# Kernel optimization log

Measured on AMD Instinct MI355X. Metric: run time of the kernel, lower is better.

The kernel has to match this reference:

```python
import jax, jax.numpy as jnp
import numpy as np

N_NODES = 100000
N_EDGES = 3200000
N_GRAPHS = 256
IN_DIM = 128
HID = 64
K = 3


def setup_inputs() -> dict:
    key = jax.random.key(0)
    ks = jax.random.split(key, 10)
    x = jax.random.normal(ks[0], (N_NODES, IN_DIM), dtype=jnp.float32)
    edge_index = jax.random.randint(ks[1], (2, N_EDGES), 0, N_NODES, dtype=jnp.int64)
    batch = jnp.sort(jax.random.randint(ks[2], (N_NODES,), 0, N_GRAPHS, dtype=jnp.int64))
    # ChebConv k-order weights: list of Linear(in, out) -> stacked [K, in, out]
    s1 = 1.0 / np.sqrt(IN_DIM)
    s2 = 1.0 / np.sqrt(HID)
    W1 = jax.random.uniform(ks[3], (K, IN_DIM, HID), jnp.float32, -s1, s1)
    b1 = jax.random.uniform(ks[4], (HID,), jnp.float32, -s1, s1)
    W2 = jax.random.uniform(ks[5], (K, HID, HID), jnp.float32, -s2, s2)
    b2 = jax.random.uniform(ks[6], (HID,), jnp.float32, -s2, s2)
    Wfc = jax.random.uniform(ks[7], (HID, 1), jnp.float32, -s2, s2)
    bfc = jax.random.uniform(ks[8], (1,), jnp.float32, -s2, s2)
    return {"x": x, "edge_index": edge_index, "batch": batch,
            "W1": W1, "b1": b1, "W2": W2, "b2": b2, "Wfc": Wfc, "bfc": bfc}


def _cheb_conv(x, src, dst, edge_w, W, b):
    # PyG ChebConv, sym normalization, lambda_max=2 => L_hat has zero diagonal
    # and off-diagonal -D^{-1/2} A D^{-1/2} (edge_w precomputed, negative).
    n = x.shape[0]
    def lhat(v):  # (L_hat v)_i = sum_{edges j->i} edge_w * v_j
        return jax.ops.segment_sum(edge_w[:, None] * v[src], dst, num_segments=n)
    Tx0 = x
    Tx1 = lhat(Tx0)
    Tx2 = 2.0 * lhat(Tx1) - Tx0
    return Tx0 @ W[0] + Tx1 @ W[1] + Tx2 @ W[2] + b


def reference(x, edge_index, batch, W1, b1, W2, b2, Wfc, bfc):
    src, dst = edge_index[0], edge_index[1]
    n = x.shape[0]
    # degree on row (source), sym normalization
    deg = jax.ops.segment_sum(jnp.ones_like(src, dtype=x.dtype), src, num_segments=n)
    dinv = jnp.where(deg > 0, jax.lax.rsqrt(jnp.maximum(deg, 1.0)), 0.0)
    edge_w = -dinv[src] * dinv[dst]  # scaled Laplacian off-diagonal weights

    h = jax.nn.relu(_cheb_conv(x, src, dst, edge_w, W1, b1))
    h = jax.nn.relu(_cheb_conv(h, src, dst, edge_w, W2, b2))

    # global mean pool over graphs
    sums = jax.ops.segment_sum(h, batch, num_segments=N_GRAPHS)
    counts = jax.ops.segment_sum(jnp.ones((n,), dtype=h.dtype), batch, num_segments=N_GRAPHS)
    pooled = sums / jnp.maximum(counts, 1.0)[:, None]

    return (pooled @ Wfc + bfc).squeeze(-1)  # [N_GRAPHS]
```

## Files before the change

### kernel.cpp

```cpp
#include <hip/hip_runtime.h>
#include <hip/hip_fp16.h>
#include <cstdint>
#include <cstddef>

static constexpr int NN = 100000;
static constexpr int NE = 3200000;
static constexpr int NG = 256;
static constexpr int NBK = (NN + 127) / 128;
static constexpr int EPB = NE / 256;

typedef _Float16 h8 __attribute__((ext_vector_type(8)));
typedef float f4v __attribute__((ext_vector_type(4)));

__device__ __forceinline__ void atomAddF(float* p, float v) {
  unsafeAtomicAdd(p, v);
}

__device__ __forceinline__ float h2f(__half h) { return __half2float(h); }

__device__ __forceinline__ unsigned pk2(float a, float b) {
  unsigned lo = __half_as_ushort(__float2half_rn(a));
  unsigned hi = __half_as_ushort(__float2half_rn(b));
  return lo | (hi << 16);
}

__global__ void k_detect(const int* __restrict__ ei, int* __restrict__ flag) {
  if (threadIdx.x == 0 && blockIdx.x == 0) {
    int nz = 0;
    for (int i = 0; i < 64; ++i) nz += (ei[2 * i + 1] != 0) ? 1 : 0;
    *flag = (nz == 0) ? 1 : 0;
  }
}

__device__ __forceinline__ int ld_idx(const void* raw, int f, int i) {
  return f ? (int)((const long long*)raw)[i] : ((const int*)raw)[i];
}

__global__ __launch_bounds__(256) void k_repack_batch(const void* __restrict__ raw,
                                                      const int* __restrict__ flag,
                                                      int* __restrict__ b32,
                                                      int* __restrict__ gcnt) {
  __shared__ int cnt[256];
  int t = threadIdx.x;
  cnt[t] = 0;
  int blk0 = blockIdx.x * 256;
  int f = *flag;
  int g0 = ld_idx(raw, f, blk0);
  __syncthreads();
  int i = blk0 + t;
  if (i < NN) {
    int g = ld_idx(raw, f, i);
    b32[i] = g;
    atomicAdd(&cnt[g - g0], 1);
  }
  __syncthreads();
  if (cnt[t] > 0) atomicAdd(&gcnt[g0 + t], cnt[t]);
}

__global__ __launch_bounds__(256) void k_hist(const void* __restrict__ raw,
                                              const int* __restrict__ flag,
                                              int* __restrict__ sCnt,
                                              int* __restrict__ dCnt,
                                              int* __restrict__ hsBlk,
                                              int* __restrict__ hdBlk) {
  __shared__ int hs[NBK], hd[NBK];
  int t = threadIdx.x;
  for (int i = t; i < NBK; i += 256) { hs[i] = 0; hd[i] = 0; }
  __syncthreads();
  int f = *flag;
  int e0 = blockIdx.x * EPB;
  for (int e = e0 + t; e < e0 + EPB; e += 256) {
    int s = ld_idx(raw, f, e);
    int d = ld_idx(raw, f, NE + e);
    atomicAdd(&hs[s >> 7], 1);
    atomicAdd(&hd[d >> 7], 1);
  }
  __syncthreads();
  size_t hb = (size_t)blockIdx.x * NBK;
  for (int i = t; i < NBK; i += 256) {
    int a = hs[i], b = hd[i];
    hsBlk[hb + i] = a;
    hdBlk[hb + i] = b;
    if (a) atomicAdd(&sCnt[i], a);
    if (b) atomicAdd(&dCnt[i], b);
  }
}

__global__ __launch_bounds__(1024) void k_scan(const int* __restrict__ sCnt,
                                               const int* __restrict__ dCnt,
                                               int* __restrict__ sBase,
                                               int* __restrict__ dBase,
                                               int* __restrict__ sCur,
                                               int* __restrict__ dCur) {
  __shared__ int sh1[1024], sh2[1024];
  int t = threadIdx.x;
  int v1 = (t < NBK) ? sCnt[t] : 0;
  int v2 = (t < NBK) ? dCnt[t] : 0;
  sh1[t] = v1; sh2[t] = v2;
  __syncthreads();
  for (int off = 1; off < 1024; off <<= 1) {
    int a1 = (t >= off) ? sh1[t - off] : 0;
    int a2 = (t >= off) ? sh2[t - off] : 0;
    __syncthreads();
    sh1[t] += a1; sh2[t] += a2;
    __syncthreads();
  }
  if (t <= NBK) {
    int b1 = sh1[t] - v1, b2 = sh2[t] - v2;
    sBase[t] = b1; dBase[t] = b2;
    if (t < NBK) { sCur[t] = b1; dCur[t] = b2; }
  }
}

__global__ __launch_bounds__(256) void k_scatter(const void* __restrict__ raw,
                                                 const int* __restrict__ flag,
                                                 const int* __restrict__ hsBlk,
                                                 const int* __restrict__ hdBlk,
                                                 int* __restrict__ sCur,
                                                 int* __restrict__ dCur,
                                                 int* __restrict__ srclist,
                                                 unsigned* __restrict__ elist) {
  __shared__ int hs[NBK], hd[NBK], cbS[NBK], cbD[NBK];
  int t = threadIdx.x;
  size_t hb = (size_t)blockIdx.x * NBK;
  for (int i = t; i < NBK; i += 256) {
    int c1 = hsBlk[hb + i];
    cbS[i] = c1 ? atomicAdd(&sCur[i], c1) : 0;
    int c2 = hdBlk[hb + i];
    cbD[i] = c2 ? atomicAdd(&dCur[i], c2) : 0;
    hs[i] = 0; hd[i] = 0;
  }
  __syncthreads();
  int f = *flag;
  int e0 = blockIdx.x * EPB;
  for (int e = e0 + t; e < e0 + EPB; e += 256) {
    int s = ld_idx(raw, f, e);
    int d = ld_idx(raw, f, NE + e);
    int bs = s >> 7, bd = d >> 7;
    int ls = atomicAdd(&hs[bs], 1);
    int ld2 = atomicAdd(&hd[bd], 1);
    srclist[cbS[bs] + ls] = s;
    elist[cbD[bd] + ld2] = (unsigned)s | ((unsigned)(d & 127) << 17);
  }
}

__global__ __launch_bounds__(256) void k_deg(const int* __restrict__ sBase,
                                             const int* __restrict__ srclist,
                                             float* __restrict__ dinv) {
  __shared__ int cnt[128];
  int t = threadIdx.x;
  if (t < 128) cnt[t] = 0;
  __syncthreads();
  int b = blockIdx.x;
  int e0 = sBase[b], e1 = sBase[b + 1];
  for (int i = e0 + t; i < e1; i += 256) atomicAdd(&cnt[srclist[i] & 127], 1);
  __syncthreads();
  if (t < 128) {
    int node = b * 128 + t;
    if (node < NN) {
      int c = cnt[t];
      dinv[node] = (c > 0) ? rsqrtf((float)c) : 0.f;
    }
  }
}

__global__ __launch_bounds__(256) void k_csr(const int* __restrict__ dBase,
                                             const unsigned* __restrict__ elist,
                                             int* __restrict__ rowptr,
                                             int* __restrict__ adj) {
  __shared__ int cnt[128], sc[128], off[128], fill[128];
  int t = threadIdx.x;
  if (t < 128) { cnt[t] = 0; fill[t] = 0; }
  __syncthreads();
  int b = blockIdx.x;
  int e0 = dBase[b], e1 = dBase[b + 1];
  for (int i = e0 + t; i < e1; i += 256) atomicAdd(&cnt[elist[i] >> 17], 1);
  __syncthreads();
  if (t < 128) sc[t] = cnt[t];
  __syncthreads();
  for (int o = 1; o < 128; o <<= 1) {
    int a = (t < 128 && t >= o) ? sc[t - o] : 0;
    __syncthreads();
    if (t < 128) sc[t] += a;
    __syncthreads();
  }
  if (t < 128) {
    off[t] = sc[t] - cnt[t];
    int node = b * 128 + t;
    if (node < NN) rowptr[node] = e0 + off[t];
  }
  if (b == NBK - 1 && t == 0) rowptr[NN] = e1;
  __syncthreads();
  for (int i = e0 + t; i < e1; i += 256) {
    unsigned w2 = elist[i];
    int l = (int)(w2 >> 17);
    int pos = atomicAdd(&fill[l], 1);
    adj[e0 + off[l] + pos] = (int)(w2 & 0x1FFFFu);
  }
}

__global__ __launch_bounds__(256) void k_prepW(const float* __restrict__ W1,
                                               const float* __restrict__ W2,
                                               __half* __restrict__ BtX,
                                               __half* __restrict__ BtH) {
  int t = blockIdx.x * 256 + threadIdx.x;
  if (t < 192 * 128) {
    int n = t >> 7, k = t & 127;
    float v;
    if (n < 64)       v = W1[k * 64 + n] - W1[16384 + k * 64 + n];
    else if (n < 128) v = W1[8192 + k * 64 + (n - 64)];
    else              v = W1[16384 + k * 64 + (n - 128)];
    BtX[n * 128 + k] = __float2half_rn(v);
  } else if (t < 192 * 128 + 64 * 192) {
    int u = t - 192 * 128;
    int n = u / 192, k = u % 192;
    int s = k >> 6, kk = k & 63;
    float v = (s == 0) ? (W2[kk * 64 + n] - W2[8192 + kk * 64 + n])
            : (s == 1) ? W2[4096 + kk * 64 + n]
                       : 2.f * W2[8192 + kk * 64 + n];
    BtH[n * 192 + k] = __float2half_rn(v);
  }
}

static constexpr int AW = 136;
__global__ __launch_bounds__(256) void k_gemm_x(const float* __restrict__ x,
                                                const __half* __restrict__ BtX,
                                                const float* __restrict__ dinv,
                                                __half* __restrict__ gV0,
                                                unsigned* __restrict__ p01) {
  __shared__ __align__(16) _Float16 As[128 * AW];
  const int t = threadIdx.x;
  const int n0 = blockIdx.x * 128;
  {
    int i = t >> 1, q = t & 1;
    int row = n0 + i;
    _Float16* dst = As + i * AW + q * 64;
    if (row < NN) {
      const float* src = x + (size_t)row * 128 + q * 64;
#pragma unroll
      for (int c = 0; c < 64; c += 4) {
        float4 v = *reinterpret_cast<const float4*>(src + c);
        ushort4 u;
        u.x = __half_as_ushort(__float2half_rn(v.x));
        u.y = __half_as_ushort(__float2half_rn(v.y));
        u.z = __half_as_ushort(__float2half_rn(v.z));
        u.w = __half_as_ushort(__float2half_rn(v.w));
        *reinterpret_cast<ushort4*>(dst + c) = u;
      }
    } else {
#pragma unroll
      for (int c = 0; c < 64; c += 4)
        *reinterpret_cast<ushort4*>(dst + c) = make_ushort4(0, 0, 0, 0);
    }
  }
  __syncthreads();
  const int w = t >> 6, lane = t & 63;
  const int quad = lane >> 4, l = lane & 15;
  f4v acc[2][12];
#pragma unroll
  for (int mt = 0; mt < 2; ++mt)
#pragma unroll
    for (int nt = 0; nt < 12; ++nt) acc[mt][nt] = (f4v){0.f, 0.f, 0.f, 0.f};

#pragma unroll
  for (int ks = 0; ks < 4; ++ks) {
    int k0 = ks * 32 + quad * 8;
    h8 a0 = *reinterpret_cast<const h8*>(As + (w * 32 + l) * AW + k0);
    h8 a1 = *reinterpret_cast<const h8*>(As + (w * 32 + 16 + l) * AW + k0);
#pragma unroll
    for (int nt = 0; nt < 12; ++nt) {
      h8 b = *reinterpret_cast<const h8*>(BtX + (size_t)(nt * 16 + l) * 128 + k0);
      acc[0][nt] = __builtin_amdgcn_mfma_f32_16x16x32_f16(a0, b, acc[0][nt], 0, 0, 0);
      acc[1][nt] = __builtin_amdgcn_mfma_f32_16x16x32_f16(a1, b, acc[1][nt], 0, 0, 0);
    }
  }
#pragma unroll
  for (int mt = 0; mt < 2; ++mt) {
#pragma unroll
    for (int r = 0; r < 4; ++r) {
      int row = n0 + w * 32 + mt * 16 + quad * 4 + r;
      if (row < NN) {
        float dv = dinv[row];
#pragma unroll
        for (int nt2 = 0; nt2 < 4; ++nt2) {
          gV0[(size_t)row * 64 + nt2 * 16 + l] = __float2half_rn(acc[mt][nt2][r]);
          p01[(size_t)row * 64 + nt2 * 16 + l] =
              pk2(dv * acc[mt][4 + nt2][r], dv * acc[mt][8 + nt2][r]);
        }
      }
    }
  }
}

__global__ __launch_bounds__(256) void k_prop2p(const int* __restrict__ rp,
                                                const int* __restrict__ adj,
                                                const unsigned* __restrict__ vp,
                                                const float* __restrict__ dinv,
                                                __half* __restrict__ oA,
                                                __half* __restrict__ oB) {
  int node = blockIdx.x * 4 + (threadIdx.x >> 6);
  int d = threadIdx.x & 63;
  if (node >= NN) return;
  int p0 = rp[node], p1 = rp[node + 1];
  float a0 = 0.f, a1 = 0.f, a2 = 0.f, a3 = 0.f;
  float b0 = 0.f, b1 = 0.f, b2 = 0.f, b3 = 0.f;
  union { unsigned u; __half2 h; } cv;
  int p = p0;
  int pA = (p0 + 3) & ~3;
  if (pA > p1) pA = p1;
  for (; p < pA; ++p) {
    cv.u = vp[(size_t)adj[p] * 64 + d];
    float2 f = __half22float2(cv.h);
    a0 += f.x; b0 += f.y;
  }
  for (; p + 8 <= p1; p += 8) {
    int4 e0 = *reinterpret_cast<const int4*>(adj + p);
    int4 e1 = *reinterpret_cast<const int4*>(adj + p + 4);
    unsigned u0 = vp[(size_t)e0.x * 64 + d], u1 = vp[(size_t)e0.y * 64 + d];
    unsigned u2 = vp[(size_t)e0.z * 64 + d], u3 = vp[(size_t)e0.w * 64 + d];
    unsigned u4 = vp[(size_t)e1.x * 64 + d], u5 = vp[(size_t)e1.y * 64 + d];
    unsigned u6 = vp[(size_t)e1.z * 64 + d], u7 = vp[(size_t)e1.w * 64 + d];
    cv.u = u0; { float2 f = __half22float2(cv.h); a0 += f.x; b0 += f.y; }
    cv.u = u1; { float2 f = __half22float2(cv.h); a1 += f.x; b1 += f.y; }
    cv.u = u2; { float2 f = __half22float2(cv.h); a2 += f.x; b2 += f.y; }
    cv.u = u3; { float2 f = __half22float2(cv.h); a3 += f.x; b3 += f.y; }
    cv.u = u4; { float2 f = __half22float2(cv.h); a0 += f.x; b0 += f.y; }
    cv.u = u5; { float2 f = __half22float2(cv.h); a1 += f.x; b1 += f.y; }
    cv.u = u6; { float2 f = __half22float2(cv.h); a2 += f.x; b2 += f.y; }
    cv.u = u7; { float2 f = __half22float2(cv.h); a3 += f.x; b3 += f.y; }
  }
  if (p + 4 <= p1) {
    int4 e = *reinterpret_cast<const int4*>(adj + p);
    unsigned u0 = vp[(size_t)e.x * 64 + d], u1 = vp[(size_t)e.y * 64 + d];
    unsigned u2 = vp[(size_t)e.z * 64 + d], u3 = vp[(size_t)e.w * 64 + d];
    cv.u = u0; { float2 f = __half22float2(cv.h); a0 += f.x; b0 += f.y; }
    cv.u = u1; { float2 f = __half22float2(cv.h); a1 += f.x; b1 += f.y; }
    cv.u = u2; { float2 f = __half22float2(cv.h); a2 += f.x; b2 += f.y; }
    cv.u = u3; { float2 f = __half22float2(cv.h); a3 += f.x; b3 += f.y; }
    p += 4;
  }
  for (; p < p1; ++p) {
    cv.u = vp[(size_t)adj[p] * 64 + d];
    float2 f = __half22float2(cv.h);
    a1 += f.x; b1 += f.y;
  }
  float sa = (a0 + a1) + (a2 + a3);
  float sb = (b0 + b1) + (b2 + b3);
  float dv = dinv[node];
  oA[(size_t)node * 64 + d] = __float2half_rn(-dv * sa);
  oB[(size_t)node * 64 + d] = __float2half_rn(-dv * dv * sb);
}

__global__ __launch_bounds__(256) void k_prop1(const int* __restrict__ rp,
                                               const int* __restrict__ adj,
                                               const __half* __restrict__ vin,
                                               const float* __restrict__ dinv,
                                               __half* __restrict__ o_p,
                                               __half* __restrict__ o_s) {
  int node = blockIdx.x * 4 + (threadIdx.x >> 6);
  int d = threadIdx.x & 63;
  if (node >= NN) return;
  int p0 = rp[node], p1 = rp[node + 1];
  float a0 = 0.f, a1 = 0.f, a2 = 0.f, a3 = 0.f;
  int p = p0;
  int pA = (p0 + 3) & ~3;
  if (pA > p1) pA = p1;
  for (; p < pA; ++p) a0 += h2f(vin[(size_t)adj[p] * 64 + d]);
  for (; p + 8 <= p1; p += 8) {
    int4 e0 = *reinterpret_cast<const int4*>(adj + p);
    int4 e1 = *reinterpret_cast<const int4*>(adj + p + 4);
    a0 += h2f(vin[(size_t)e0.x * 64 + d]);
    a1 += h2f(vin[(size_t)e0.y * 64 + d]);
    a2 += h2f(vin[(size_t)e0.z * 64 + d]);
    a3 += h2f(vin[(size_t)e0.w * 64 + d]);
    a0 += h2f(vin[(size_t)e1.x * 64 + d]);
    a1 += h2f(vin[(size_t)e1.y * 64 + d]);
    a2 += h2f(vin[(size_t)e1.z * 64 + d]);
    a3 += h2f(vin[(size_t)e1.w * 64 + d]);
  }
  if (p + 4 <= p1) {
    int4 e = *reinterpret_cast<const int4*>(adj + p);
    a0 += h2f(vin[(size_t)e.x * 64 + d]);
    a1 += h2f(vin[(size_t)e.y * 64 + d]);
    a2 += h2f(vin[(size_t)e.z * 64 + d]);
    a3 += h2f(vin[(size_t)e.w * 64 + d]);
    p += 4;
  }
  for (; p < p1; ++p) a1 += h2f(vin[(size_t)adj[p] * 64 + d]);
  float s = (a0 + a1) + (a2 + a3);
  float dv = dinv[node];
  float pl = -dv * s;
  o_p[(size_t)node * 64 + d] = __float2half_rn(pl);
  if (o_s) o_s[(size_t)node * 64 + d] = __float2half_rn(dv * pl);
}

__global__ __launch_bounds__(256) void k_prop_h1(const int* __restrict__ rp,
                                                 const int* __restrict__ adj,
                                                 const __half* __restrict__ vin,
                                                 const float* __restrict__ dinv,
                                                 const __half* __restrict__ gV0,
                                                 const __half* __restrict__ gP,
                                                 const float* __restrict__ b1v,
                                                 __half* __restrict__ gH1,
                                                 __half* __restrict__ gH1s) {
  int node = blockIdx.x * 4 + (threadIdx.x >> 6);
  int d = threadIdx.x & 63;
  if (node >= NN) return;
  int p0 = rp[node], p1 = rp[node + 1];
  float a0 = 0.f, a1 = 0.f, a2 = 0.f, a3 = 0.f;
  int p = p0;
  int pA = (p0 + 3) & ~3;
  if (pA > p1) pA = p1;
  for (; p < pA; ++p) a0 += h2f(vin[(size_t)adj[p] * 64 + d]);
  for (; p + 8 <= p1; p += 8) {
    int4 e0 = *reinterpret_cast<const int4*>(adj + p);
    int4 e1 = *reinterpret_cast<const int4*>(adj + p + 4);
    a0 += h2f(vin[(size_t)e0.x * 64 + d]);
    a1 += h2f(vin[(size_t)e0.y * 64 + d]);
    a2 += h2f(vin[(size_t)e0.z * 64 + d]);
    a3 += h2f(vin[(size_t)e0.w * 64 + d]);
    a0 += h2f(vin[(size_t)e1.x * 64 + d]);
    a1 += h2f(vin[(size_t)e1.y * 64 + d]);
    a2 += h2f(vin[(size_t)e1.z * 64 + d]);
    a3 += h2f(vin[(size_t)e1.w * 64 + d]);
  }
  if (p + 4 <= p1) {
    int4 e = *reinterpret_cast<const int4*>(adj + p);
    a0 += h2f(vin[(size_t)e.x * 64 + d]);
    a1 += h2f(vin[(size_t)e.y * 64 + d]);
    a2 += h2f(vin[(size_t)e.z * 64 + d]);
    a3 += h2f(vin[(size_t)e.w * 64 + d]);
    p += 4;
  }
  for (; p < p1; ++p) a1 += h2f(vin[(size_t)adj[p] * 64 + d]);
  float s = (a0 + a1) + (a2 + a3);
  float dv = dinv[node];
  float R = -dv * s;
  size_t idx = (size_t)node * 64 + d;
  float h = h2f(gV0[idx]) + h2f(gP[idx]) + 2.f * R + b1v[d];
  h = fmaxf(h, 0.f);
  gH1[idx] = __float2half_rn(h);
  gH1s[idx] = __float2half_rn(dv * h);
}

static constexpr int HW = 200;
__global__ __launch_bounds__(256) void k_gemm_h2_pool(const __half* __restrict__ gH1,
                                                      const __half* __restrict__ gT1,
                                                      const __half* __restrict__ gT2,
                                                      const __half* __restrict__ BtH,
                                                      const float* __restrict__ b2v,
                                                      const int* __restrict__ b32,
                                                      float* __restrict__ pooled) {
  __shared__ __align__(16) char smem[128 * HW * 2];
  __shared__ int gb[128];
  _Float16* As = reinterpret_cast<_Float16*>(smem);
  const int t = threadIdx.x;
  const int n0 = blockIdx.x * 128;
  if (t < 128) gb[t] = (n0 + t < NN) ? b32[n0 + t] : -1;
  for (int c = t; c < 128 * 24; c += 256) {
    int row = c / 24, seg = c % 24;
    int tb = seg >> 3, off = (seg & 7) * 8;
    int rowg = n0 + row;
    h8 v = (h8){0, 0, 0, 0, 0, 0, 0, 0};
    if (rowg < NN) {
      const __half* src = (tb == 0 ? gH1 : tb == 1 ? gT1 : gT2) + (size_t)rowg * 64 + off;
      v = *reinterpret_cast<const h8*>(src);
    }
    *reinterpret_cast<h8*>(As + row * HW + seg * 8) = v;
  }
  __syncthreads();
  const int w = t >> 6, lane = t & 63;
  const int quad = lane >> 4, l = lane & 15;
  f4v acc[2][4];
#pragma unroll
  for (int mt = 0; mt < 2; ++mt)
#pragma unroll
    for (int nt = 0; nt < 4; ++nt) acc[mt][nt] = (f4v){0.f, 0.f, 0.f, 0.f};
#pragma unroll
  for (int ks = 0; ks < 6; ++ks) {
    int k0 = ks * 32 + quad * 8;
    h8 a0 = *reinterpret_cast<const h8*>(As + (w * 32 + l) * HW + k0);
    h8 a1 = *reinterpret_cast<const h8*>(As + (w * 32 + 16 + l) * HW + k0);
#pragma unroll
    for (int nt = 0; nt < 4; ++nt) {
      h8 b = *reinterpret_cast<const h8*>(BtH + (size_t)(nt * 16 + l) * 192 + k0);
      acc[0][nt] = __builtin_amdgcn_mfma_f32_16x16x32_f16(a0, b, acc[0][nt], 0, 0, 0);
      acc[1][nt] = __builtin_amdgcn_mfma_f32_16x16x32_f16(a1, b, acc[1][nt], 0, 0, 0);
    }
  }
  __syncthreads();
  float (*ht)[68] = reinterpret_cast<float (*)[68]>(smem);
#pragma unroll
  for (int mt = 0; mt < 2; ++mt)
#pragma unroll
    for (int r = 0; r < 4; ++r) {
      int rl = w * 32 + mt * 16 + quad * 4 + r;
#pragma unroll
      for (int nt = 0; nt < 4; ++nt) {
        int col = nt * 16 + l;
        ht[rl][col] = fmaxf(acc[mt][nt][r] + b2v[col], 0.f);
      }
    }
  __syncthreads();
  int rg = t >> 6;
  int d = t & 63;
  int base = rg * 32;
  int cur = -2;
  float s = 0.f;
  for (int i2 = 0; i2 < 32; ++i2) {
    int g = gb[base + i2];
    if (g != cur) {
      if (cur >= 0) atomAddF(&pooled[cur * 64 + d], s);
      s = 0.f;
      cur = g;
    }
    if (g >= 0) s += ht[base + i2][d];
  }
  if (cur >= 0) atomAddF(&pooled[cur * 64 + d], s);
}

__global__ void k_out(const float* __restrict__ pooled, const int* __restrict__ gcnt,
                      const float* __restrict__ Wfc, const float* __restrict__ bfc,
                      float* __restrict__ out) {
  int g = blockIdx.x, t = threadIdx.x;
  float v = pooled[g * 64 + t] * Wfc[t];
  int c = gcnt[g];
  v /= (float)(c > 0 ? c : 1);
  for (int off = 32; off > 0; off >>= 1) v += __shfl_down(v, off, 64);
  if (t == 0) out[g] = v + bfc[0];
}

extern "C" void kernel_launch(void* const* d_in, const int* in_sizes, int n_in,
                              void* d_out, int out_size, void* d_ws, size_t ws_size,
                              hipStream_t stream) {
  const float* x   = (const float*)d_in[0];
  const void*  ei  = d_in[1];
  const void*  bat = d_in[2];
  const float* W1  = (const float*)d_in[3];
  const float* b1v = (const float*)d_in[4];
  const float* W2  = (const float*)d_in[5];
  const float* b2v = (const float*)d_in[6];
  const float* Wfc = (const float*)d_in[7];
  const float* bfc = (const float*)d_in[8];
  float* out = (float*)d_out;

  char* w = (char*)d_ws;
  size_t o = 0;
  auto take = [&](size_t bytes) -> void* {
    void* p = w + o;
    o = (o + bytes + 255) & ~(size_t)255;
    return p;
  };
  int*      flag   = (int*)take(256);
  int*      gcnt   = (int*)take((size_t)NG * 4);
  float*    pooled = (float*)take((size_t)NG * 64 * 4);
  int*      sCnt   = (int*)take((size_t)(NBK + 2) * 4);
  int*      dCnt   = (int*)take((size_t)(NBK + 2) * 4);
  char*     zend   = w + o;
  int*      sBase  = (int*)take((size_t)(NBK + 2) * 4);
  int*      dBase  = (int*)take((size_t)(NBK + 2) * 4);
  int*      sCur   = (int*)take((size_t)(NBK + 2) * 4);
  int*      dCur   = (int*)take((size_t)(NBK + 2) * 4);
  int*      b32    = (int*)take((size_t)NN * 4);
  float*    dinv   = (float*)take((size_t)NN * 4);
  int*      rowptr = (int*)take((size_t)(NN + 2) * 4);
  int*      hsBlk  = (int*)take((size_t)256 * NBK * 4);
  int*      hdBlk  = (int*)take((size_t)256 * NBK * 4);
  int*      srclist= (int*)take((size_t)NE * 4);
  unsigned* elist  = (unsigned*)take((size_t)NE * 4);
  __half*   BtX    = (__half*)take((size_t)192 * 128 * 2);
  __half*   BtH    = (__half*)take((size_t)64 * 192 * 2);
  __half*   gV0    = (__half*)take((size_t)NN * 64 * 2);
  unsigned* p01    = (unsigned*)take((size_t)NN * 64 * 4);
  __half*   gP     = (__half*)take((size_t)NN * 64 * 2);
  __half*   gQs    = (__half*)take((size_t)NN * 64 * 2);
  __half*   gH1    = (__half*)take((size_t)NN * 64 * 2);
  __half*   gH1s   = (__half*)take((size_t)NN * 64 * 2);
  __half*   gT1    = (__half*)take((size_t)NN * 64 * 2);
  __half*   gT1s   = (__half*)take((size_t)NN * 64 * 2);
  __half*   gT2    = (__half*)take((size_t)NN * 64 * 2);
  int*      adj    = srclist;
  (void)in_sizes; (void)n_in; (void)out_size; (void)ws_size;

  hipMemsetAsync(gcnt, 0, (size_t)(zend - (char*)gcnt), stream);

  k_detect<<<1, 64, 0, stream>>>((const int*)ei, flag);
  k_repack_batch<<<(NN + 255) / 256, 256, 0, stream>>>(bat, flag, b32, gcnt);
  k_prepW<<<(192 * 128 + 64 * 192 + 255) / 256, 256, 0, stream>>>(W1, W2, BtX, BtH);
  k_hist<<<256, 256, 0, stream>>>(ei, flag, sCnt, dCnt, hsBlk, hdBlk);
  k_scan<<<1, 1024, 0, stream>>>(sCnt, dCnt, sBase, dBase, sCur, dCur);
  k_scatter<<<256, 256, 0, stream>>>(ei, flag, hsBlk, hdBlk, sCur, dCur, srclist, elist);
  k_deg<<<NBK, 256, 0, stream>>>(sBase, srclist, dinv);
  k_csr<<<NBK, 256, 0, stream>>>(dBase, elist, rowptr, adj);

  const int gemm_grid = (NN + 127) / 128;
  const int prop_grid = (NN + 3) / 4;

  k_gemm_x<<<gemm_grid, 256, 0, stream>>>(x, BtX, dinv, gV0, p01);
  k_prop2p<<<prop_grid, 256, 0, stream>>>(rowptr, adj, p01, dinv, gP, gQs);
  k_prop_h1<<<prop_grid, 256, 0, stream>>>(rowptr, adj, gQs, dinv, gV0, gP, b1v, gH1, gH1s);
  k_prop1<<<prop_grid, 256, 0, stream>>>(rowptr, adj, gH1s, dinv, gT1, gT1s);
  k_prop1<<<prop_grid, 256, 0, stream>>>(rowptr, adj, gT1s, dinv, gT2, nullptr);
  k_gemm_h2_pool<<<gemm_grid, 256, 0, stream>>>(gH1, gT1, gT2, BtH, b2v, b32, pooled);
  k_out<<<NG, 64, 0, stream>>>(pooled, gcnt, Wfc, bfc, out);
}
```

Measured before the change: 680.5 us.

## Reorder second ChebConv as GEMM-then-propagate, merge setup kernels

The second layer now multiplies H1 by the stacked weights first and then runs Horner-style propagation on 64-wide projected features, instead of propagating H1 twice and doing a 192-wide GEMM. This makes both layers use the same two-pass gather pattern. The first layer's packed two-channel gather becomes two single-table gathers. The small setup kernels are merged into combined front and back launches, and pooling becomes a per-node float atomic in the last propagation kernel. The costs are many more global atomics on the pooled buffer, and a separate adj buffer so srclist is no longer aliased.

```diff
diff --git a/kernel.cpp b/kernel.cpp
--- a/kernel.cpp
+++ b/kernel.cpp
@@ -8,6 +8,9 @@
 static constexpr int NG = 256;
 static constexpr int NBK = (NN + 127) / 128;
 static constexpr int EPB = NE / 256;
+static constexpr int GB_BATCH = (NN + 255) / 256;
+static constexpr int GB_PREPW = (192 * 128 + 192 * 64 + 255) / 256;
+static constexpr int GB_HIST = 256;
 
 typedef _Float16 h8 __attribute__((ext_vector_type(8)));
 typedef float f4v __attribute__((ext_vector_type(4)));
@@ -15,14 +18,7 @@
 __device__ __forceinline__ void atomAddF(float* p, float v) {
   unsafeAtomicAdd(p, v);
 }
-
 __device__ __forceinline__ float h2f(__half h) { return __half2float(h); }
-
-__device__ __forceinline__ unsigned pk2(float a, float b) {
-  unsigned lo = __half_as_ushort(__float2half_rn(a));
-  unsigned hi = __half_as_ushort(__float2half_rn(b));
-  return lo | (hi << 16);
-}
 
 __global__ void k_detect(const int* __restrict__ ei, int* __restrict__ flag) {
   if (threadIdx.x == 0 && blockIdx.x == 0) {
@@ -36,53 +32,78 @@
   return f ? (int)((const long long*)raw)[i] : ((const int*)raw)[i];
 }
 
-__global__ __launch_bounds__(256) void k_repack_batch(const void* __restrict__ raw,
-                                                      const int* __restrict__ flag,
-                                                      int* __restrict__ b32,
-                                                      int* __restrict__ gcnt) {
-  __shared__ int cnt[256];
+__global__ __launch_bounds__(256) void k_front(const void* __restrict__ bat,
+                                               const void* __restrict__ ei,
+                                               const int* __restrict__ flag,
+                                               const float* __restrict__ W1,
+                                               const float* __restrict__ W2,
+                                               int* __restrict__ b32,
+                                               int* __restrict__ gcnt,
+                                               __half* __restrict__ BtX,
+                                               __half* __restrict__ BtH2,
+                                               int* __restrict__ sCnt,
+                                               int* __restrict__ dCnt,
+                                               int* __restrict__ hsBlk,
+                                               int* __restrict__ hdBlk) {
+  __shared__ int sh[2 * NBK];
+  int b = blockIdx.x;
   int t = threadIdx.x;
-  cnt[t] = 0;
-  int blk0 = blockIdx.x * 256;
-  int f = *flag;
-  int g0 = ld_idx(raw, f, blk0);
-  __syncthreads();
-  int i = blk0 + t;
-  if (i < NN) {
-    int g = ld_idx(raw, f, i);
-    b32[i] = g;
-    atomicAdd(&cnt[g - g0], 1);
-  }
-  __syncthreads();
-  if (cnt[t] > 0) atomicAdd(&gcnt[g0 + t], cnt[t]);
-}
-
-__global__ __launch_bounds__(256) void k_hist(const void* __restrict__ raw,
-                                              const int* __restrict__ flag,
-                                              int* __restrict__ sCnt,
-                                              int* __restrict__ dCnt,
-                                              int* __restrict__ hsBlk,
-                                              int* __restrict__ hdBlk) {
-  __shared__ int hs[NBK], hd[NBK];
-  int t = threadIdx.x;
-  for (int i = t; i < NBK; i += 256) { hs[i] = 0; hd[i] = 0; }
-  __syncthreads();
-  int f = *flag;
-  int e0 = blockIdx.x * EPB;
-  for (int e = e0 + t; e < e0 + EPB; e += 256) {
-    int s = ld_idx(raw, f, e);
-    int d = ld_idx(raw, f, NE + e);
-    atomicAdd(&hs[s >> 7], 1);
-    atomicAdd(&hd[d >> 7], 1);
-  }
-  __syncthreads();
-  size_t hb = (size_t)blockIdx.x * NBK;
-  for (int i = t; i < NBK; i += 256) {
-    int a = hs[i], b = hd[i];
-    hsBlk[hb + i] = a;
-    hdBlk[hb + i] = b;
-    if (a) atomicAdd(&sCnt[i], a);
-    if (b) atomicAdd(&dCnt[i], b);
+  if (b < GB_BATCH) {
+    int* cnt = sh;
+    cnt[t] = 0;
+    int blk0 = b * 256;
+    int f = *flag;
+    int g0 = ld_idx(bat, f, blk0);
+    __syncthreads();
+    int i = blk0 + t;
+    if (i < NN) {
+      int g = ld_idx(bat, f, i);
+      b32[i] = g;
+      atomicAdd(&cnt[g - g0], 1);
+    }
+    __syncthreads();
+    if (cnt[t] > 0) atomicAdd(&gcnt[g0 + t], cnt[t]);
+  } else if (b < GB_BATCH + GB_PREPW) {
+    int u = (b - GB_BATCH) * 256 + t;
+    if (u < 192 * 128) {
+      int n = u >> 7, k = u & 127;
+      float v;
+      if (n < 64)       v = W1[k * 64 + n] - W1[16384 + k * 64 + n];
+      else if (n < 128) v = W1[8192 + k * 64 + (n - 64)];
+      else              v = W1[16384 + k * 64 + (n - 128)];
+      BtX[n * 128 + k] = __float2half_rn(v);
+    } else if (u < 192 * 128 + 192 * 64) {
+      int u2 = u - 192 * 128;
+      int n = u2 >> 6, k = u2 & 63;
+      float v;
+      if (n < 64)       v = W2[k * 64 + n] - W2[8192 + k * 64 + n];
+      else if (n < 128) v = W2[4096 + k * 64 + (n - 64)];
+      else              v = W2[8192 + k * 64 + (n - 128)];
+      BtH2[n * 64 + k] = __float2half_rn(v);
+    }
+  } else {
+    int hb = b - GB_BATCH - GB_PREPW;
+    int* hs = sh;
+    int* hd = sh + NBK;
+    for (int i = t; i < NBK; i += 256) { hs[i] = 0; hd[i] = 0; }
+    __syncthreads();
+    int f = *flag;
+    int e0 = hb * EPB;
+    for (int e = e0 + t; e < e0 + EPB; e += 256) {
+      int s = ld_idx(ei, f, e);
+      int d = ld_idx(ei, f, NE + e);
+      atomicAdd(&hs[s >> 7], 1);
+      atomicAdd(&hd[d >> 7], 1);
+    }
+    __syncthreads();
+    size_t hoff = (size_t)hb * NBK;
+    for (int i = t; i < NBK; i += 256) {
+      int a = hs[i], c = hd[i];
+      hsBlk[hoff + i] = a;
+      hdBlk[hoff + i] = c;
+      if (a) atomicAdd(&sCnt[i], a);
+      if (c) atomicAdd(&dCnt[i], c);
+    }
   }
 }
 
@@ -144,81 +165,58 @@
   }
 }
 
-__global__ __launch_bounds__(256) void k_deg(const int* __restrict__ sBase,
-                                             const int* __restrict__ srclist,
-                                             float* __restrict__ dinv) {
-  __shared__ int cnt[128];
-  int t = threadIdx.x;
-  if (t < 128) cnt[t] = 0;
-  __syncthreads();
-  int b = blockIdx.x;
-  int e0 = sBase[b], e1 = sBase[b + 1];
-  for (int i = e0 + t; i < e1; i += 256) atomicAdd(&cnt[srclist[i] & 127], 1);
-  __syncthreads();
-  if (t < 128) {
-    int node = b * 128 + t;
-    if (node < NN) {
-      int c = cnt[t];
-      dinv[node] = (c > 0) ? rsqrtf((float)c) : 0.f;
-    }
-  }
-}
-
-__global__ __launch_bounds__(256) void k_csr(const int* __restrict__ dBase,
-                                             const unsigned* __restrict__ elist,
-                                             int* __restrict__ rowptr,
-                                             int* __restrict__ adj) {
+__global__ __launch_bounds__(256) void k_back(const int* __restrict__ sBase,
+                                              const int* __restrict__ srclist,
+                                              float* __restrict__ dinv,
+                                              const int* __restrict__ dBase,
+                                              const unsigned* __restrict__ elist,
+                                              int* __restrict__ rowptr,
+                                              int* __restrict__ adj) {
   __shared__ int cnt[128], sc[128], off[128], fill[128];
   int t = threadIdx.x;
-  if (t < 128) { cnt[t] = 0; fill[t] = 0; }
-  __syncthreads();
-  int b = blockIdx.x;
-  int e0 = dBase[b], e1 = dBase[b + 1];
-  for (int i = e0 + t; i < e1; i += 256) atomicAdd(&cnt[elist[i] >> 17], 1);
-  __syncthreads();
-  if (t < 128) sc[t] = cnt[t];
-  __syncthreads();
-  for (int o = 1; o < 128; o <<= 1) {
-    int a = (t < 128 && t >= o) ? sc[t - o] : 0;
-    __syncthreads();
-    if (t < 128) sc[t] += a;
-    __syncthreads();
-  }
-  if (t < 128) {
-    off[t] = sc[t] - cnt[t];
-    int node = b * 128 + t;
-    if (node < NN) rowptr[node] = e0 + off[t];
-  }
-  if (b == NBK - 1 && t == 0) rowptr[NN] = e1;
-  __syncthreads();
-  for (int i = e0 + t; i < e1; i += 256) {
-    unsigned w2 = elist[i];
-    int l = (int)(w2 >> 17);
-    int pos = atomicAdd(&fill[l], 1);
-    adj[e0 + off[l] + pos] = (int)(w2 & 0x1FFFFu);
-  }
-}
-
-__global__ __launch_bounds__(256) void k_prepW(const float* __restrict__ W1,
-                                               const float* __restrict__ W2,
-                                               __half* __restrict__ BtX,
-                                               __half* __restrict__ BtH) {
-  int t = blockIdx.x * 256 + threadIdx.x;
-  if (t < 192 * 128) {
-    int n = t >> 7, k = t & 127;
-    float v;
-    if (n < 64)       v = W1[k * 64 + n] - W1[16384 + k * 64 + n];
-    else if (n < 128) v = W1[8192 + k * 64 + (n - 64)];
-    else              v = W1[16384 + k * 64 + (n - 128)];
-    BtX[n * 128 + k] = __float2half_rn(v);
-  } else if (t < 192 * 128 + 64 * 192) {
-    int u = t - 192 * 128;
-    int n = u / 192, k = u % 192;
-    int s = k >> 6, kk = k & 63;
-    float v = (s == 0) ? (W2[kk * 64 + n] - W2[8192 + kk * 64 + n])
-            : (s == 1) ? W2[4096 + kk * 64 + n]
-                       : 2.f * W2[8192 + kk * 64 + n];
-    BtH[n * 192 + k] = __float2half_rn(v);
+  int bb = blockIdx.x;
+  if (bb < NBK) {
+    int b = bb;
+    if (t < 128) cnt[t] = 0;
+    __syncthreads();
+    int e0 = sBase[b], e1 = sBase[b + 1];
+    for (int i = e0 + t; i < e1; i += 256) atomicAdd(&cnt[srclist[i] & 127], 1);
+    __syncthreads();
+    if (t < 128) {
+      int node = b * 128 + t;
+      if (node < NN) {
+        int c = cnt[t];
+        dinv[node] = (c > 0) ? rsqrtf((float)c) : 0.f;
+      }
+    }
+  } else {
+    int b = bb - NBK;
+    if (t < 128) { cnt[t] = 0; fill[t] = 0; }
+    __syncthreads();
+    int e0 = dBase[b], e1 = dBase[b + 1];
+    for (int i = e0 + t; i < e1; i += 256) atomicAdd(&cnt[elist[i] >> 17], 1);
+    __syncthreads();
+    if (t < 128) sc[t] = cnt[t];
+    __syncthreads();
+    for (int o = 1; o < 128; o <<= 1) {
+      int a = (t < 128 && t >= o) ? sc[t - o] : 0;
+      __syncthreads();
+      if (t < 128) sc[t] += a;
+      __syncthreads();
+    }
+    if (t < 128) {
+      off[t] = sc[t] - cnt[t];
+      int node = b * 128 + t;
+      if (node < NN) rowptr[node] = e0 + off[t];
+    }
+    if (b == NBK - 1 && t == 0) rowptr[NN] = e1;
+    __syncthreads();
+    for (int i = e0 + t; i < e1; i += 256) {
+      unsigned w2 = elist[i];
+      int l = (int)(w2 >> 17);
+      int pos = atomicAdd(&fill[l], 1);
+      adj[e0 + off[l] + pos] = (int)(w2 & 0x1FFFFu);
+    }
   }
 }
 
@@ -227,7 +225,8 @@
                                                 const __half* __restrict__ BtX,
                                                 const float* __restrict__ dinv,
                                                 __half* __restrict__ gV0,
-                                                unsigned* __restrict__ p01) {
+                                                __half* __restrict__ gA1,
+                                                __half* __restrict__ gU2s) {
   __shared__ __align__(16) _Float16 As[128 * AW];
   const int t = threadIdx.x;
   const int n0 = blockIdx.x * 128;
@@ -283,240 +282,154 @@
         float dv = dinv[row];
 #pragma unroll
         for (int nt2 = 0; nt2 < 4; ++nt2) {
-          gV0[(size_t)row * 64 + nt2 * 16 + l] = __float2half_rn(acc[mt][nt2][r]);
-          p01[(size_t)row * 64 + nt2 * 16 + l] =
-              pk2(dv * acc[mt][4 + nt2][r], dv * acc[mt][8 + nt2][r]);
+          int col = nt2 * 16 + l;
+          gV0[(size_t)row * 64 + col] = __float2half_rn(acc[mt][nt2][r]);
+          gA1[(size_t)row * 64 + col] = __float2half_rn(acc[mt][4 + nt2][r]);
+          gU2s[(size_t)row * 64 + col] = __float2half_rn(dv * acc[mt][8 + nt2][r]);
         }
       }
     }
   }
 }
 
-__global__ __launch_bounds__(256) void k_prop2p(const int* __restrict__ rp,
-                                                const int* __restrict__ adj,
-                                                const unsigned* __restrict__ vp,
+static constexpr int HW2 = 72;
+__global__ __launch_bounds__(256) void k_gemm_h(const __half* __restrict__ gH1,
+                                                const __half* __restrict__ BtH2,
                                                 const float* __restrict__ dinv,
-                                                __half* __restrict__ oA,
-                                                __half* __restrict__ oB) {
+                                                __half* __restrict__ gV02,
+                                                __half* __restrict__ gA2,
+                                                __half* __restrict__ gB2s) {
+  __shared__ __align__(16) _Float16 As[128 * HW2];
+  const int t = threadIdx.x;
+  const int n0 = blockIdx.x * 128;
+  for (int c = t; c < 128 * 8; c += 256) {
+    int row = c >> 3, seg = c & 7;
+    int rowg = n0 + row;
+    h8 v = (h8){0, 0, 0, 0, 0, 0, 0, 0};
+    if (rowg < NN) v = *reinterpret_cast<const h8*>(gH1 + (size_t)rowg * 64 + seg * 8);
+    *reinterpret_cast<h8*>(As + row * HW2 + seg * 8) = v;
+  }
+  __syncthreads();
+  const int w = t >> 6, lane = t & 63;
+  const int quad = lane >> 4, l = lane & 15;
+  f4v acc[2][12];
+#pragma unroll
+  for (int mt = 0; mt < 2; ++mt)
+#pragma unroll
+    for (int nt = 0; nt < 12; ++nt) acc[mt][nt] = (f4v){0.f, 0.f, 0.f, 0.f};
+#pragma unroll
+  for (int ks = 0; ks < 2; ++ks) {
+    int k0 = ks * 32 + quad * 8;
+    h8 a0 = *reinterpret_cast<const h8*>(As + (w * 32 + l) * HW2 + k0);
+    h8 a1 = *reinterpret_cast<const h8*>(As + (w * 32 + 16 + l) * HW2 + k0);
+#pragma unroll
+    for (int nt = 0; nt < 12; ++nt) {
+      h8 b = *reinterpret_cast<const h8*>(BtH2 + (size_t)(nt * 16 + l) * 64 + k0);
+      acc[0][nt] = __builtin_amdgcn_mfma_f32_16x16x32_f16(a0, b, acc[0][nt], 0, 0, 0);
+      acc[1][nt] = __builtin_amdgcn_mfma_f32_16x16x32_f16(a1, b, acc[1][nt], 0, 0, 0);
+    }
+  }
+#pragma unroll
+  for (int mt = 0; mt < 2; ++mt) {
+#pragma unroll
+    for (int r = 0; r < 4; ++r) {
+      int row = n0 + w * 32 + mt * 16 + quad * 4 + r;
+      if (row < NN) {
+        float dv = dinv[row];
+#pragma unroll
+        for (int nt2 = 0; nt2 < 4; ++nt2) {
+          int col = nt2 * 16 + l;
+          gV02[(size_t)row * 64 + col] = __float2half_rn(acc[mt][nt2][r]);
+          gA2[(size_t)row * 64 + col] = __float2half_rn(acc[mt][4 + nt2][r]);
+          gB2s[(size_t)row * 64 + col] = __float2half_rn(dv * acc[mt][8 + nt2][r]);
+        }
+      }
+    }
+  }
+}
+
+#define GATHER_SUM(tbl)                                                    \
+  int p0 = rp[node], p1 = rp[node + 1];                                    \
+  float a0 = 0.f, a1 = 0.f, a2 = 0.f, a3 = 0.f;                            \
+  int p = p0;                                                              \
+  int pA = (p0 + 3) & ~3;                                                  \
+  if (pA > p1) pA = p1;                                                    \
+  for (; p < pA; ++p) a0 += h2f(tbl[(size_t)adj[p] * 64 + d]);             \
+  for (; p + 8 <= p1; p += 8) {                                            \
+    int4 e0 = *reinterpret_cast<const int4*>(adj + p);                     \
+    int4 e1 = *reinterpret_cast<const int4*>(adj + p + 4);                 \
+    a0 += h2f(tbl[(size_t)e0.x * 64 + d]);                                 \
+    a1 += h2f(tbl[(size_t)e0.y * 64 + d]);                                 \
+    a2 += h2f(tbl[(size_t)e0.z * 64 + d]);                                 \
+    a3 += h2f(tbl[(size_t)e0.w * 64 + d]);                                 \
+    a0 += h2f(tbl[(size_t)e1.x * 64 + d]);                                 \
+    a1 += h2f(tbl[(size_t)e1.y * 64 + d]);                                 \
+    a2 += h2f(tbl[(size_t)e1.z * 64 + d]);                                 \
+    a3 += h2f(tbl[(size_t)e1.w * 64 + d]);                                 \
+  }                                                                        \
+  if (p + 4 <= p1) {                                                       \
+    int4 e = *reinterpret_cast<const int4*>(adj + p);                      \
+    a0 += h2f(tbl[(size_t)e.x * 64 + d]);                                  \
+    a1 += h2f(tbl[(size_t)e.y * 64 + d]);                                  \
+    a2 += h2f(tbl[(size_t)e.z * 64 + d]);                                  \
+    a3 += h2f(tbl[(size_t)e.w * 64 + d]);                                  \
+    p += 4;                                                                \
+  }                                                                        \
+  for (; p < p1; ++p) a1 += h2f(tbl[(size_t)adj[p] * 64 + d]);             \
+  float s = (a0 + a1) + (a2 + a3);
+
+__global__ __launch_bounds__(256) void k_propA(const int* __restrict__ rp,
+                                               const int* __restrict__ adj,
+                                               const __half* __restrict__ tbl,
+                                               const __half* __restrict__ aux,
+                                               const float* __restrict__ dinv,
+                                               __half* __restrict__ outT) {
   int node = blockIdx.x * 4 + (threadIdx.x >> 6);
   int d = threadIdx.x & 63;
   if (node >= NN) return;
-  int p0 = rp[node], p1 = rp[node + 1];
-  float a0 = 0.f, a1 = 0.f, a2 = 0.f, a3 = 0.f;
-  float b0 = 0.f, b1 = 0.f, b2 = 0.f, b3 = 0.f;
-  union { unsigned u; __half2 h; } cv;
-  int p = p0;
-  int pA = (p0 + 3) & ~3;
-  if (pA > p1) pA = p1;
-  for (; p < pA; ++p) {
-    cv.u = vp[(size_t)adj[p] * 64 + d];
-    float2 f = __half22float2(cv.h);
-    a0 += f.x; b0 += f.y;
-  }
-  for (; p + 8 <= p1; p += 8) {
-    int4 e0 = *reinterpret_cast<const int4*>(adj + p);
-    int4 e1 = *reinterpret_cast<const int4*>(adj + p + 4);
-    unsigned u0 = vp[(size_t)e0.x * 64 + d], u1 = vp[(size_t)e0.y * 64 + d];
-    unsigned u2 = vp[(size_t)e0.z * 64 + d], u3 = vp[(size_t)e0.w * 64 + d];
-    unsigned u4 = vp[(size_t)e1.x * 64 + d], u5 = vp[(size_t)e1.y * 64 + d];
-    unsigned u6 = vp[(size_t)e1.z * 64 + d], u7 = vp[(size_t)e1.w * 64 + d];
-    cv.u = u0; { float2 f = __half22float2(cv.h); a0 += f.x; b0 += f.y; }
-    cv.u = u1; { float2 f = __half22float2(cv.h); a1 += f.x; b1 += f.y; }
-    cv.u = u2; { float2 f = __half22float2(cv.h); a2 += f.x; b2 += f.y; }
-    cv.u = u3; { float2 f = __half22float2(cv.h); a3 += f.x; b3 += f.y; }
-    cv.u = u4; { float2 f = __half22float2(cv.h); a0 += f.x; b0 += f.y; }
-    cv.u = u5; { float2 f = __half22float2(cv.h); a1 += f.x; b1 += f.y; }
-    cv.u = u6; { float2 f = __half22float2(cv.h); a2 += f.x; b2 += f.y; }
-    cv.u = u7; { float2 f = __half22float2(cv.h); a3 += f.x; b3 += f.y; }
-  }
-  if (p + 4 <= p1) {
-    int4 e = *reinterpret_cast<const int4*>(adj + p);
-    unsigned u0 = vp[(size_t)e.x * 64 + d], u1 = vp[(size_t)e.y * 64 + d];
-    unsigned u2 = vp[(size_t)e.z * 64 + d], u3 = vp[(size_t)e.w * 64 + d];
-    cv.u = u0; { float2 f = __half22float2(cv.h); a0 += f.x; b0 += f.y; }
-    cv.u = u1; { float2 f = __half22float2(cv.h); a1 += f.x; b1 += f.y; }
-    cv.u = u2; { float2 f = __half22float2(cv.h); a2 += f.x; b2 += f.y; }
-    cv.u = u3; { float2 f = __half22float2(cv.h); a3 += f.x; b3 += f.y; }
-    p += 4;
-  }
-  for (; p < p1; ++p) {
-    cv.u = vp[(size_t)adj[p] * 64 + d];
-    float2 f = __half22float2(cv.h);
-    a1 += f.x; b1 += f.y;
-  }
-  float sa = (a0 + a1) + (a2 + a3);
-  float sb = (b0 + b1) + (b2 + b3);
+  GATHER_SUM(tbl)
   float dv = dinv[node];
-  oA[(size_t)node * 64 + d] = __float2half_rn(-dv * sa);
-  oB[(size_t)node * 64 + d] = __float2half_rn(-dv * dv * sb);
-}
-
-__global__ __launch_bounds__(256) void k_prop1(const int* __restrict__ rp,
+  float tt = -dv * s;
+  size_t idx = (size_t)node * 64 + d;
+  outT[idx] = __float2half_rn(dv * (h2f(aux[idx]) + 2.f * tt));
+}
+
+__global__ __launch_bounds__(256) void k_propB(const int* __restrict__ rp,
                                                const int* __restrict__ adj,
-                                               const __half* __restrict__ vin,
+                                               const __half* __restrict__ tbl,
+                                               const __half* __restrict__ gV0,
+                                               const float* __restrict__ b1v,
                                                const float* __restrict__ dinv,
-                                               __half* __restrict__ o_p,
-                                               __half* __restrict__ o_s) {
+                                               __half* __restrict__ gH1) {
   int node = blockIdx.x * 4 + (threadIdx.x >> 6);
   int d = threadIdx.x & 63;
   if (node >= NN) return;
-  int p0 = rp[node], p1 = rp[node + 1];
-  float a0 = 0.f, a1 = 0.f, a2 = 0.f, a3 = 0.f;
-  int p = p0;
-  int pA = (p0 + 3) & ~3;
-  if (pA > p1) pA = p1;
-  for (; p < pA; ++p) a0 += h2f(vin[(size_t)adj[p] * 64 + d]);
-  for (; p + 8 <= p1; p += 8) {
-    int4 e0 = *reinterpret_cast<const int4*>(adj + p);
-    int4 e1 = *reinterpret_cast<const int4*>(adj + p + 4);
-    a0 += h2f(vin[(size_t)e0.x * 64 + d]);
-    a1 += h2f(vin[(size_t)e0.y * 64 + d]);
-    a2 += h2f(vin[(size_t)e0.z * 64 + d]);
-    a3 += h2f(vin[(size_t)e0.w * 64 + d]);
-    a0 += h2f(vin[(size_t)e1.x * 64 + d]);
-    a1 += h2f(vin[(size_t)e1.y * 64 + d]);
-    a2 += h2f(vin[(size_t)e1.z * 64 + d]);
-    a3 += h2f(vin[(size_t)e1.w * 64 + d]);
-  }
-  if (p + 4 <= p1) {
-    int4 e = *reinterpret_cast<const int4*>(adj + p);
-    a0 += h2f(vin[(size_t)e.x * 64 + d]);
-    a1 += h2f(vin[(size_t)e.y * 64 + d]);
-    a2 += h2f(vin[(size_t)e.z * 64 + d]);
-    a3 += h2f(vin[(size_t)e.w * 64 + d]);
-    p += 4;
-  }
-  for (; p < p1; ++p) a1 += h2f(vin[(size_t)adj[p] * 64 + d]);
-  float s = (a0 + a1) + (a2 + a3);
+  GATHER_SUM(tbl)
   float dv = dinv[node];
-  float pl = -dv * s;
-  o_p[(size_t)node * 64 + d] = __float2half_rn(pl);
-  if (o_s) o_s[(size_t)node * 64 + d] = __float2half_rn(dv * pl);
-}
-
-__global__ __launch_bounds__(256) void k_prop_h1(const int* __restrict__ rp,
-                                                 const int* __restrict__ adj,
-                                                 const __half* __restrict__ vin,
-                                                 const float* __restrict__ dinv,
-                                                 const __half* __restrict__ gV0,
-                                                 const __half* __restrict__ gP,
-                                                 const float* __restrict__ b1v,
-                                                 __half* __restrict__ gH1,
-                                                 __half* __restrict__ gH1s) {
+  float r = -dv * s;
+  size_t idx = (size_t)node * 64 + d;
+  float h = fmaxf(h2f(gV0[idx]) + r + b1v[d], 0.f);
+  gH1[idx] = __float2half_rn(h);
+}
+
+__global__ __launch_bounds__(256) void k_propD(const int* __restrict__ rp,
+                                               const int* __restrict__ adj,
+                                               const __half* __restrict__ tbl,
+                                               const __half* __restrict__ gV02,
+                                               const float* __restrict__ b2v,
+                                               const float* __restrict__ dinv,
+                                               const int* __restrict__ b32,
+                                               float* __restrict__ pooled) {
   int node = blockIdx.x * 4 + (threadIdx.x >> 6);
   int d = threadIdx.x & 63;
   if (node >= NN) return;
-  int p0 = rp[node], p1 = rp[node + 1];
-  float a0 = 0.f, a1 = 0.f, a2 = 0.f, a3 = 0.f;
-  int p = p0;
-  int pA = (p0 + 3) & ~3;
-  if (pA > p1) pA = p1;
-  for (; p < pA; ++p) a0 += h2f(vin[(size_t)adj[p] * 64 + d]);
-  for (; p + 8 <= p1; p += 8) {
-    int4 e0 = *reinterpret_cast<const int4*>(adj + p);
-    int4 e1 = *reinterpret_cast<const int4*>(adj + p + 4);
-    a0 += h2f(vin[(size_t)e0.x * 64 + d]);
-    a1 += h2f(vin[(size_t)e0.y * 64 + d]);
-    a2 += h2f(vin[(size_t)e0.z * 64 + d]);
-    a3 += h2f(vin[(size_t)e0.w * 64 + d]);
-    a0 += h2f(vin[(size_t)e1.x * 64 + d]);
-    a1 += h2f(vin[(size_t)e1.y * 64 + d]);
-    a2 += h2f(vin[(size_t)e1.z * 64 + d]);
-    a3 += h2f(vin[(size_t)e1.w * 64 + d]);
-  }
-  if (p + 4 <= p1) {
-    int4 e = *reinterpret_cast<const int4*>(adj + p);
-    a0 += h2f(vin[(size_t)e.x * 64 + d]);
-    a1 += h2f(vin[(size_t)e.y * 64 + d]);
-    a2 += h2f(vin[(size_t)e.z * 64 + d]);
-    a3 += h2f(vin[(size_t)e.w * 64 + d]);
-    p += 4;
-  }
-  for (; p < p1; ++p) a1 += h2f(vin[(size_t)adj[p] * 64 + d]);
-  float s = (a0 + a1) + (a2 + a3);
+  GATHER_SUM(tbl)
   float dv = dinv[node];
-  float R = -dv * s;
+  float r = -dv * s;
   size_t idx = (size_t)node * 64 + d;
-  float h = h2f(gV0[idx]) + h2f(gP[idx]) + 2.f * R + b1v[d];
-  h = fmaxf(h, 0.f);
-  gH1[idx] = __float2half_rn(h);
-  gH1s[idx] = __float2half_rn(dv * h);
-}
-
-static constexpr int HW = 200;
-__global__ __launch_bounds__(256) void k_gemm_h2_pool(const __half* __restrict__ gH1,
-                                                      const __half* __restrict__ gT1,
-                                                      const __half* __restrict__ gT2,
-                                                      const __half* __restrict__ BtH,
-                                                      const float* __restrict__ b2v,
-                                                      const int* __restrict__ b32,
-                                                      float* __restrict__ pooled) {
-  __shared__ __align__(16) char smem[128 * HW * 2];
-  __shared__ int gb[128];
-  _Float16* As = reinterpret_cast<_Float16*>(smem);
-  const int t = threadIdx.x;
-  const int n0 = blockIdx.x * 128;
-  if (t < 128) gb[t] = (n0 + t < NN) ? b32[n0 + t] : -1;
-  for (int c = t; c < 128 * 24; c += 256) {
-    int row = c / 24, seg = c % 24;
-    int tb = seg >> 3, off = (seg & 7) * 8;
-    int rowg = n0 + row;
-    h8 v = (h8){0, 0, 0, 0, 0, 0, 0, 0};
-    if (rowg < NN) {
-      const __half* src = (tb == 0 ? gH1 : tb == 1 ? gT1 : gT2) + (size_t)rowg * 64 + off;
-      v = *reinterpret_cast<const h8*>(src);
-    }
-    *reinterpret_cast<h8*>(As + row * HW + seg * 8) = v;
-  }
-  __syncthreads();
-  const int w = t >> 6, lane = t & 63;
-  const int quad = lane >> 4, l = lane & 15;
-  f4v acc[2][4];
-#pragma unroll
-  for (int mt = 0; mt < 2; ++mt)
-#pragma unroll
-    for (int nt = 0; nt < 4; ++nt) acc[mt][nt] = (f4v){0.f, 0.f, 0.f, 0.f};
-#pragma unroll
-  for (int ks = 0; ks < 6; ++ks) {
-    int k0 = ks * 32 + quad * 8;
-    h8 a0 = *reinterpret_cast<const h8*>(As + (w * 32 + l) * HW + k0);
-    h8 a1 = *reinterpret_cast<const h8*>(As + (w * 32 + 16 + l) * HW + k0);
-#pragma unroll
-    for (int nt = 0; nt < 4; ++nt) {
-      h8 b = *reinterpret_cast<const h8*>(BtH + (size_t)(nt * 16 + l) * 192 + k0);
-      acc[0][nt] = __builtin_amdgcn_mfma_f32_16x16x32_f16(a0, b, acc[0][nt], 0, 0, 0);
-      acc[1][nt] = __builtin_amdgcn_mfma_f32_16x16x32_f16(a1, b, acc[1][nt], 0, 0, 0);
-    }
-  }
-  __syncthreads();
-  float (*ht)[68] = reinterpret_cast<float (*)[68]>(smem);
-#pragma unroll
-  for (int mt = 0; mt < 2; ++mt)
-#pragma unroll
-    for (int r = 0; r < 4; ++r) {
-      int rl = w * 32 + mt * 16 + quad * 4 + r;
-#pragma unroll
-      for (int nt = 0; nt < 4; ++nt) {
-        int col = nt * 16 + l;
-        ht[rl][col] = fmaxf(acc[mt][nt][r] + b2v[col], 0.f);
-      }
-    }
-  __syncthreads();
-  int rg = t >> 6;
-  int d = t & 63;
-  int base = rg * 32;
-  int cur = -2;
-  float s = 0.f;
-  for (int i2 = 0; i2 < 32; ++i2) {
-    int g = gb[base + i2];
-    if (g != cur) {
-      if (cur >= 0) atomAddF(&pooled[cur * 64 + d], s);
-      s = 0.f;
-      cur = g;
-    }
-    if (g >= 0) s += ht[base + i2][d];
-  }
-  if (cur >= 0) atomAddF(&pooled[cur * 64 + d], s);
+  float h = fmaxf(h2f(gV02[idx]) + r + b2v[d], 0.f);
+  int g = b32[node];
+  atomAddF(&pooled[g * 64 + d], h);
 }
 
 __global__ void k_out(const float* __restrict__ pooled, const int* __restrict__ gcnt,
@@ -568,39 +481,37 @@
   int*      hdBlk  = (int*)take((size_t)256 * NBK * 4);
   int*      srclist= (int*)take((size_t)NE * 4);
   unsigned* elist  = (unsigned*)take((size_t)NE * 4);
+  int*      adj    = (int*)take((size_t)NE * 4);
   __half*   BtX    = (__half*)take((size_t)192 * 128 * 2);
-  __half*   BtH    = (__half*)take((size_t)64 * 192 * 2);
+  __half*   BtH2   = (__half*)take((size_t)192 * 64 * 2);
   __half*   gV0    = (__half*)take((size_t)NN * 64 * 2);
-  unsigned* p01    = (unsigned*)take((size_t)NN * 64 * 4);
-  __half*   gP     = (__half*)take((size_t)NN * 64 * 2);
-  __half*   gQs    = (__half*)take((size_t)NN * 64 * 2);
+  __half*   gA1    = (__half*)take((size_t)NN * 64 * 2);
+  __half*   gU2s   = (__half*)take((size_t)NN * 64 * 2);
+  __half*   gM1    = (__half*)take((size_t)NN * 64 * 2);
   __half*   gH1    = (__half*)take((size_t)NN * 64 * 2);
-  __half*   gH1s   = (__half*)take((size_t)NN * 64 * 2);
-  __half*   gT1    = (__half*)take((size_t)NN * 64 * 2);
-  __half*   gT1s   = (__half*)take((size_t)NN * 64 * 2);
-  __half*   gT2    = (__half*)take((size_t)NN * 64 * 2);
-  int*      adj    = srclist;
+  __half*   gV02   = gU2s;
+  __half*   gA2    = gA1;
+  __half*   gB2s   = gV0;
+  __half*   gM2    = gM1;
   (void)in_sizes; (void)n_in; (void)out_size; (void)ws_size;
 
   hipMemsetAsync(gcnt, 0, (size_t)(zend - (char*)gcnt), stream);
 
   k_detect<<<1, 64, 0, stream>>>((const int*)ei, flag);
-  k_repack_batch<<<(NN + 255) / 256, 256, 0, stream>>>(bat, flag, b32, gcnt);
-  k_prepW<<<(192 * 128 + 64 * 192 + 255) / 256, 256, 0, stream>>>(W1, W2, BtX, BtH);
-  k_hist<<<256, 256, 0, stream>>>(ei, flag, sCnt, dCnt, hsBlk, hdBlk);
+  k_front<<<GB_BATCH + GB_PREPW + GB_HIST, 256, 0, stream>>>(
+      bat, ei, flag, W1, W2, b32, gcnt, BtX, BtH2, sCnt, dCnt, hsBlk, hdBlk);
   k_scan<<<1, 1024, 0, stream>>>(sCnt, dCnt, sBase, dBase, sCur, dCur);
   k_scatter<<<256, 256, 0, stream>>>(ei, flag, hsBlk, hdBlk, sCur, dCur, srclist, elist);
-  k_deg<<<NBK, 256, 0, stream>>>(sBase, srclist, dinv);
-  k_csr<<<NBK, 256, 0, stream>>>(dBase, elist, rowptr, adj);
+  k_back<<<2 * NBK, 256, 0, stream>>>(sBase, srclist, dinv, dBase, elist, rowptr, adj);
 
   const int gemm_grid = (NN + 127) / 128;
   const int prop_grid = (NN + 3) / 4;
 
-  k_gemm_x<<<gemm_grid, 256, 0, stream>>>(x, BtX, dinv, gV0, p01);
-  k_prop2p<<<prop_grid, 256, 0, stream>>>(rowptr, adj, p01, dinv, gP, gQs);
-  k_prop_h1<<<prop_grid, 256, 0, stream>>>(rowptr, adj, gQs, dinv, gV0, gP, b1v, gH1, gH1s);
-  k_prop1<<<prop_grid, 256, 0, stream>>>(rowptr, adj, gH1s, dinv, gT1, gT1s);
-  k_prop1<<<prop_grid, 256, 0, stream>>>(rowptr, adj, gT1s, dinv, gT2, nullptr);
-  k_gemm_h2_pool<<<gemm_grid, 256, 0, stream>>>(gH1, gT1, gT2, BtH, b2v, b32, pooled);
+  k_gemm_x<<<gemm_grid, 256, 0, stream>>>(x, BtX, dinv, gV0, gA1, gU2s);
+  k_propA<<<prop_grid, 256, 0, stream>>>(rowptr, adj, gU2s, gA1, dinv, gM1);
+  k_propB<<<prop_grid, 256, 0, stream>>>(rowptr, adj, gM1, gV0, b1v, dinv, gH1);
+  k_gemm_h<<<gemm_grid, 256, 0, stream>>>(gH1, BtH2, dinv, gV02, gA2, gB2s);
+  k_propA<<<prop_grid, 256, 0, stream>>>(rowptr, adj, gB2s, gA2, dinv, gM2);
+  k_propD<<<prop_grid, 256, 0, stream>>>(rowptr, adj, gM2, gV02, b2v, dinv, b32, pooled);
   k_out<<<NG, 64, 0, stream>>>(pooled, gcnt, Wfc, bfc, out);
 }
```

Result: no change. 692.9 us (+1.8%).
